# Optimization experiments

Measured on AMD Instinct MI355X. Metric: run time of the kernel, lower is better.

Reference implementation:

```python
import jax, jax.numpy as jnp
import numpy as np


def setup_inputs() -> dict:
    key = jax.random.key(0)
    k1, k2, k3 = jax.random.split(key, 3)
    x = jax.random.normal(k1, (1, 512, 14, 14), dtype=jnp.float32)
    w1 = jax.random.normal(k2, (16, 64, 3), dtype=jnp.float32)
    w2 = jax.random.normal(k3, (32, 8, 3), dtype=jnp.float32)
    return {"x": x, "w1": w1, "w2": w2}


def reference(x, w1, w2):
    SHIFT = 1  # module picks +/-1 at random init; fixed to +1
    H = W = 14
    # reshape (1,512,14,14) -> (1, i=64, o=8, H, W), roll along H
    xr = x.reshape(1, 64, 8, H, W)
    xr = jnp.roll(xr, SHIFT, axis=3)
    # unfold with kernel (3,1), pad (1,0) along H == stack 3 shifted slices
    xp = jnp.pad(xr, ((0, 0), (0, 0), (0, 0), (1, 1), (0, 0)))
    t3 = jnp.stack([xp[:, :, :, j:j + H, :] for j in range(3)], axis=3)  # (1,64,8,3,14,14)
    # conv 1: contract i=64 channels and j=3 taps per group o -> k=16 outputs
    t4 = jnp.einsum('liojmn,kij->lkomn', t3, w1)  # (1,16,8,14,14)
    # unfold with kernel (3,1), pad (1,0) along W (after the (1,1792,14,1) reshape)
    tp = jnp.pad(t4, ((0, 0), (0, 0), (0, 0), (0, 0), (1, 1)))
    t5 = jnp.stack([tp[..., k:k + W] for k in range(3)], axis=4)  # (1,16,8,14,3,14)
    # conv 2: contract j=8 group channels and k=3 taps -> i=32 outputs per o=16
    t6 = jnp.einsum('lojmkn,ijk->liomn', t5, w2)  # (1,32,16,14,14)
    return t6.reshape(1, 512, H, W)
```

## Files before the change

kernel.cpp:

```cpp
#include <hip/hip_runtime.h>


__global__ __launch_bounds__(512) void fused_shift_conv(
    const float* __restrict__ x,
    const float* __restrict__ w1,
    const float* __restrict__ w2,
    float* __restrict__ out)
{
    const int bx = blockIdx.x;
    const int m  = bx >> 4;
    const int o2 = bx & 15;
    const int t  = threadIdx.x;

    __shared__ float w2s[32 * 8 * 3];
    __shared__ float t4s[112];

    if (t < 224) {
        const int quarter = t & 3;
        const int r  = t >> 2;
        const int o  = r / 7;
        const int n0 = (r % 7) * 2;
        const int ibase = quarter * 16;

        float4 w1v[12];
        {
            const float4* w1p = (const float4*)(w1 + (size_t)o2 * 192 + ibase * 3);
            #pragma unroll
            for (int q = 0; q < 12; ++q) w1v[q] = w1p[q];
        }

        float2 xv[3][16];
        #pragma unroll
        for (int j = 0; j < 3; ++j) {
            const int hp = m + j - 1;
            if (hp >= 0 && hp < 14) {
                const int row = (hp + 13) % 14;
                const float* xp = x + (size_t)(ibase * 8 + o) * 196 + row * 14 + n0;
                #pragma unroll
                for (int i = 0; i < 16; ++i)
                    xv[j][i] = *(const float2*)(xp + (size_t)i * 8 * 196);
            } else {
                #pragma unroll
                for (int i = 0; i < 16; ++i) xv[j][i] = make_float2(0.f, 0.f);
            }
        }

        float2 acc = make_float2(0.f, 0.f);
        const float* w1f = (const float*)w1v;
        #pragma unroll
        for (int j = 0; j < 3; ++j) {
            #pragma unroll
            for (int i = 0; i < 16; ++i) {
                const float w = w1f[i * 3 + j];
                acc.x += xv[j][i].x * w;
                acc.y += xv[j][i].y * w;
            }
        }

        acc.x += __shfl_xor(acc.x, 1);
        acc.y += __shfl_xor(acc.y, 1);
        acc.x += __shfl_xor(acc.x, 2);
        acc.y += __shfl_xor(acc.y, 2);
        if (quarter == 0) *(float2*)(t4s + o * 14 + n0) = acc;
    } else if (t >= 320) {
        ((float4*)w2s)[t - 320] = ((const float4*)w2)[t - 320];
    }

    __syncthreads();

    if (t < 448) {
        const int n  = t % 14;
        const int i2 = t / 14;
        const float* wp = w2s + i2 * 24;
        float acc = 0.f;
        #pragma unroll
        for (int j = 0; j < 8; ++j) {
            const float* tp = t4s + j * 14;
            #pragma unroll
            for (int k = 0; k < 3; ++k) {
                const int nn = n + k - 1;
                if (nn >= 0 && nn < 14) acc += tp[nn] * wp[j * 3 + k];
            }
        }
        out[((size_t)(i2 * 16 + o2) * 14 + m) * 14 + n] = acc;
    }
}

extern "C" void kernel_launch(void* const* d_in, const int* in_sizes, int n_in,
                              void* d_out, int out_size, void* d_ws, size_t ws_size,
                              hipStream_t stream) {
    const float* x  = (const float*)d_in[0];
    const float* w1 = (const float*)d_in[1];
    const float* w2 = (const float*)d_in[2];
    float* out = (float*)d_out;
    fused_shift_conv<<<dim3(224), dim3(512), 0, stream>>>(x, w1, w2, out);
}
```

Baseline: 63.51 us.

## Use all 448 threads for stage one and defer quarter reduction to stage two

Stage one now runs on all 448 threads, one output element each, instead of 224 threads each doing two elements. The four partial sums over input-channel quarters go to shared memory as float4 rather than being combined with wave shuffles, and stage two sums them while it convolves. The w2 weights are loaded straight into registers, so the shared-memory staging copy is gone. This is meant to raise parallelism in the latency-bound first stage and drop the shuffle reduction, at the cost of four times more shared-memory reads in stage two and more registers per thread.

```diff
diff --git a/kernel.cpp b/kernel.cpp
--- a/kernel.cpp
+++ b/kernel.cpp
@@ -1,7 +1,7 @@
 #include <hip/hip_runtime.h>
 
 
-__global__ __launch_bounds__(512) void fused_shift_conv(
+__global__ __launch_bounds__(448) void fused_shift_conv(
     const float* __restrict__ x,
     const float* __restrict__ w1,
     const float* __restrict__ w2,
@@ -12,78 +12,74 @@
     const int o2 = bx & 15;
     const int t  = threadIdx.x;
 
-    __shared__ float w2s[32 * 8 * 3];
-    __shared__ float t4s[112];
+    __shared__ float t4p[112][4];
 
-    if (t < 224) {
-        const int quarter = t & 3;
-        const int r  = t >> 2;
-        const int o  = r / 7;
-        const int n0 = (r % 7) * 2;
-        const int ibase = quarter * 16;
+    const int quarter = t / 112;
+    const int r = t % 112;
+    const int o = r / 14;
+    const int n = t % 14;
+    const int ibase = quarter * 16;
+    const int i2 = t / 14;
 
-        float4 w1v[12];
-        {
-            const float4* w1p = (const float4*)(w1 + (size_t)o2 * 192 + ibase * 3);
+    float4 w2v[6];
+    {
+        const float4* w2p = (const float4*)(w2 + (size_t)i2 * 24);
+        #pragma unroll
+        for (int q = 0; q < 6; ++q) w2v[q] = w2p[q];
+    }
+
+    float4 w1v[12];
+    {
+        const float4* w1p = (const float4*)(w1 + (size_t)o2 * 192 + ibase * 3);
+        #pragma unroll
+        for (int q = 0; q < 12; ++q) w1v[q] = w1p[q];
+    }
+
+    float xv[3][16];
+    #pragma unroll
+    for (int j = 0; j < 3; ++j) {
+        const int hp = m + j - 1;
+        if (hp >= 0 && hp < 14) {
+            const int row = (hp + 13) % 14;
+            const float* xp = x + (size_t)(ibase * 8 + o) * 196 + row * 14 + n;
             #pragma unroll
-            for (int q = 0; q < 12; ++q) w1v[q] = w1p[q];
+            for (int i = 0; i < 16; ++i)
+                xv[j][i] = xp[(size_t)i * 8 * 196];
+        } else {
+            #pragma unroll
+            for (int i = 0; i < 16; ++i) xv[j][i] = 0.f;
         }
+    }
 
-        float2 xv[3][16];
+    float acc1 = 0.f;
+    const float* w1f = (const float*)w1v;
+    #pragma unroll
+    for (int j = 0; j < 3; ++j) {
         #pragma unroll
-        for (int j = 0; j < 3; ++j) {
-            const int hp = m + j - 1;
-            if (hp >= 0 && hp < 14) {
-                const int row = (hp + 13) % 14;
-                const float* xp = x + (size_t)(ibase * 8 + o) * 196 + row * 14 + n0;
-                #pragma unroll
-                for (int i = 0; i < 16; ++i)
-                    xv[j][i] = *(const float2*)(xp + (size_t)i * 8 * 196);
-            } else {
-                #pragma unroll
-                for (int i = 0; i < 16; ++i) xv[j][i] = make_float2(0.f, 0.f);
-            }
+        for (int i = 0; i < 16; ++i) {
+            acc1 += xv[j][i] * w1f[i * 3 + j];
         }
-
-        float2 acc = make_float2(0.f, 0.f);
-        const float* w1f = (const float*)w1v;
-        #pragma unroll
-        for (int j = 0; j < 3; ++j) {
-            #pragma unroll
-            for (int i = 0; i < 16; ++i) {
-                const float w = w1f[i * 3 + j];
-                acc.x += xv[j][i].x * w;
-                acc.y += xv[j][i].y * w;
-            }
-        }
-
-        acc.x += __shfl_xor(acc.x, 1);
-        acc.y += __shfl_xor(acc.y, 1);
-        acc.x += __shfl_xor(acc.x, 2);
-        acc.y += __shfl_xor(acc.y, 2);
-        if (quarter == 0) *(float2*)(t4s + o * 14 + n0) = acc;
-    } else if (t >= 320) {
-        ((float4*)w2s)[t - 320] = ((const float4*)w2)[t - 320];
     }
+    t4p[r][quarter] = acc1;
 
     __syncthreads();
 
-    if (t < 448) {
-        const int n  = t % 14;
-        const int i2 = t / 14;
-        const float* wp = w2s + i2 * 24;
-        float acc = 0.f;
+    const float* w2f = (const float*)w2v;
+    float4 a4 = make_float4(0.f, 0.f, 0.f, 0.f);
+    #pragma unroll
+    for (int j = 0; j < 8; ++j) {
         #pragma unroll
-        for (int j = 0; j < 8; ++j) {
-            const float* tp = t4s + j * 14;
-            #pragma unroll
-            for (int k = 0; k < 3; ++k) {
-                const int nn = n + k - 1;
-                if (nn >= 0 && nn < 14) acc += tp[nn] * wp[j * 3 + k];
+        for (int k = 0; k < 3; ++k) {
+            const int nn = n + k - 1;
+            if (nn >= 0 && nn < 14) {
+                const float4 p = *(const float4*)t4p[j * 14 + nn];
+                const float w = w2f[j * 3 + k];
+                a4.x += p.x * w; a4.y += p.y * w;
+                a4.z += p.z * w; a4.w += p.w * w;
             }
         }
-        out[((size_t)(i2 * 16 + o2) * 14 + m) * 14 + n] = acc;
     }
+    out[((size_t)(i2 * 16 + o2) * 14 + m) * 14 + n] = (a4.x + a4.y) + (a4.z + a4.w);
 }
 
 extern "C" void kernel_launch(void* const* d_in, const int* in_sizes, int n_in,
@@ -93,5 +89,5 @@
     const float* w1 = (const float*)d_in[1];
     const float* w2 = (const float*)d_in[2];
     float* out = (float*)d_out;
-    fused_shift_conv<<<dim3(224), dim3(512), 0, stream>>>(x, w1, w2, out);
+    fused_shift_conv<<<dim3(224), dim3(448), 0, stream>>>(x, w1, w2, out);
 }
```

Measured after the change: 60.26 us. 5.1% less time.
